# Kernel tuning notes

Measured on AMD Instinct MI355X. Metric: run time of the kernel, lower is better.

The kernel has to match this reference:

```python
import jax, jax.numpy as jnp
from jax import lax
import numpy as np

B = 16384
D = 32
N_HEADS = 4


def _piece_table():
    base = np.zeros((7, 4, 4), np.int32)
    cells = [
        [(1, 0), (1, 1), (1, 2), (1, 3)],  # I
        [(1, 1), (1, 2), (2, 1), (2, 2)],  # O
        [(1, 1), (2, 0), (2, 1), (2, 2)],  # T
        [(1, 1), (1, 2), (2, 0), (2, 1)],  # S
        [(1, 0), (1, 1), (2, 1), (2, 2)],  # Z
        [(1, 0), (2, 0), (2, 1), (2, 2)],  # J
        [(1, 2), (2, 0), (2, 1), (2, 2)],  # L
    ]
    for i, cs in enumerate(cells):
        for (r, c) in cs:
            base[i, r, c] = 1
    rots = np.stack([np.stack([np.rot90(base[i], k) for k in range(4)]) for i in range(7)])
    p = np.concatenate([rots, np.zeros((1, 4, 4, 4), np.int32)], 0)  # [8,4,4,4]
    return jnp.asarray(p)


def setup_inputs() -> dict:
    key = jax.random.key(0)
    ks = jax.random.split(key, 24)

    def ri(k, n, lo, hi):
        return jax.random.randint(k, (B, n), lo, hi, dtype=jnp.int32)

    t = jnp.concatenate([
        ri(ks[0], 1, 0, 10),   # col0 feature
        ri(ks[1], 1, 2, 8),
        ri(ks[2], 1, 0, 10),   # col2 y pos
        ri(ks[3], 1, 0, 8),    # col3 drop dist
        ri(ks[4], 1, 0, 4),    # col4 rotation
        ri(ks[5], 3, 0, 10),   # cols5-7
        ri(ks[6], 1, 0, 7),    # col8 piece id
        ri(ks[7], 6, 0, 7),    # cols9-14 hold/next
        ri(ks[8], 7, 0, 10),   # cols15-21
        ri(ks[9], 210, 0, 2),  # cols22-231 board
    ], axis=1)

    s = 0.05
    rn = lambda k, shp: jax.random.normal(k, shp, jnp.float32) * s
    return {
        "t": t,
        "piece_table": _piece_table(),
        "conv1_w": rn(ks[10], (6, 3, 5, 5)), "conv1_b": rn(ks[11], (6,)),
        "conv2_w": rn(ks[12], (16, 6, 5, 5)), "conv2_b": rn(ks[13], (16,)),
        "conv3_w": rn(ks[14], (64, 16, 3, 1)), "conv3_b": rn(ks[15], (64,)),
        "lfc1_w": rn(ks[16], (32, 64)), "lfc1_b": rn(ks[17], (32,)),
        "fc_w": rn(ks[18], (32, 8)), "fc_b": rn(ks[19], (32,)),
        "emb": rn(ks[20], (8, D)),
        "in_proj_w": rn(ks[21], (3 * D, D)), "in_proj_b": jnp.zeros((3 * D,), jnp.float32),
        "out_proj_w": rn(ks[22], (D, D)), "out_proj_b": jnp.zeros((D,), jnp.float32),
    }


def _avgpool2(x):
    b, c, h, w = x.shape
    h2, w2 = h // 2, w // 2
    return x[:, :, :h2 * 2, :w2 * 2].reshape(b, c, h2, 2, w2, 2).mean((3, 5))


def _lenet(x, w1, b1, w2, b2, w3, b3, fw, fb):
    dn = ("NCHW", "OIHW", "NCHW")
    x = jax.nn.relu(lax.conv_general_dilated(x, w1, (1, 1), ((2, 2), (2, 2)), dimension_numbers=dn) + b1[None, :, None, None])
    x = _avgpool2(x)                                   # [B,6,11,6]
    x = jax.nn.relu(lax.conv_general_dilated(x, w2, (1, 1), ((0, 0), (0, 0)), dimension_numbers=dn) + b2[None, :, None, None])
    x = _avgpool2(x)                                   # [B,16,3,1]
    x = jax.nn.relu(lax.conv_general_dilated(x, w3, (1, 1), ((0, 0), (0, 0)), dimension_numbers=dn) + b3[None, :, None, None])
    x = x.reshape(-1, 64)
    return jax.nn.relu(x @ fw.T + fb)                  # [B,32]


def _pe():
    pos = jnp.array([0, 0, 1, 2, 3, 4, 5], jnp.float32)[:, None]
    div = jnp.exp(jnp.arange(0, D, 2, dtype=jnp.float32) * (-jnp.log(10000.0) / D))
    s, c = jnp.sin(pos * div), jnp.cos(pos * div)      # [7,16] each
    return jnp.stack([s, c], -1).reshape(7, D)         # interleaved sin/cos


def _mha(q_in, kv, in_w, in_b, out_w, out_b):
    qw, kw, vw = in_w[:D], in_w[D:2 * D], in_w[2 * D:]
    qb, kb, vb = in_b[:D], in_b[D:2 * D], in_b[2 * D:]
    b, lq, _ = q_in.shape
    hd = D // N_HEADS
    q = (q_in @ qw.T + qb).reshape(b, lq, N_HEADS, hd)
    k = (kv @ kw.T + kb).reshape(b, -1, N_HEADS, hd)
    v = (kv @ vw.T + vb).reshape(b, -1, N_HEADS, hd)
    scores = jnp.einsum("bqhd,bkhd->bhqk", q, k) / jnp.sqrt(jnp.float32(hd))
    w = jax.nn.softmax(scores, axis=-1)
    o = jnp.einsum("bhqk,bkhd->bqhd", w, v).reshape(b, lq, D)
    return o @ out_w.T + out_b


def reference(t, piece_table, conv1_w, conv1_b, conv2_w, conv2_b, conv3_w, conv3_b,
              lfc1_w, lfc1_b, fc_w, fc_b, emb, in_proj_w, in_proj_b, out_proj_w, out_proj_b):
    bsz = t.shape[0]
    board = jnp.zeros((bsz, 3, 21, 10), jnp.float32)
    board = board.at[:, 0].set(t[:, 22:232].astype(jnp.float32).reshape(bsz, 21, 10))

    # gather piece grid, extract the 4 filled cells per sample in row-major order
    pieces = piece_table[t[:, 8], t[:, 4]].reshape(bsz, 16)        # [B,16] in {0,1}
    idx = jnp.argsort(1 - pieces, axis=1, stable=True)[:, :4]      # first 4 ones, scan order
    cy, cx = idx // 4, idx % 4
    x = cx + t[:, 1][:, None] - 2
    y = cy + t[:, 2][:, None]
    ny = y + t[:, 3][:, None]
    mask = (y >= 0) & (ny >= 0)
    br = jnp.arange(bsz, dtype=jnp.int32)[:, None]
    y_m = jnp.where(mask, y, -1)
    ny_m = jnp.where(mask, ny, -1)
    board = board.at[br, 1, y_m, x].set(1.0, mode="drop")
    board = board.at[br, 2, ny_m, x].set(1.0, mode="drop")

    board = jnp.pad(board, ((0, 0), (0, 0), (0, 1), (1, 1)), constant_values=1.0)  # [B,3,22,12]

    t9 = jnp.where((t[:, 9] != -1) & (t[:, 6] != 0), t[:, 9], 7)
    hold_next = jnp.concatenate([t[:, 8:9], t9[:, None], t[:, 10:15]], axis=1)     # [B,7]

    b2 = _lenet(board, conv1_w, conv1_b, conv2_w, conv2_b, conv3_w, conv3_b, lfc1_w, lfc1_b)  # [B,32]
    bkv = b2[:, None, :]                                            # [B,1,32]
    p = emb[hold_next] + _pe()[None]                                # [B,7,32]
    a = _mha(p, bkv, in_proj_w, in_proj_b, out_proj_w, out_proj_b)  # [B,7,32]

    xf = jax.nn.relu(t[:, :8].astype(jnp.float32) @ fc_w.T + fc_b)  # [B,32]
    out = jnp.concatenate([xf, a.mean(axis=1), b2], axis=1)         # [B,96]
    return (out, board)
```

## Files before the change

kernel.cpp:

```cpp
#include <hip/hip_runtime.h>
#include <cstddef>


#define BATCH 16384
#define SPB   4
#define NBLK  (BATCH / SPB)
#define SS    1804

__global__ __launch_bounds__(256, 4)
void board_model_kernel(const int* __restrict__ t,
                        const int* __restrict__ piece_table,
                        const float* __restrict__ w1, const float* __restrict__ b1,
                        const float* __restrict__ w2, const float* __restrict__ b2w,
                        const float* __restrict__ w3, const float* __restrict__ b3,
                        const float* __restrict__ wf1, const float* __restrict__ bf1,
                        const float* __restrict__ fcw, const float* __restrict__ fcb,
                        const float* __restrict__ ipw, const float* __restrict__ ipb,
                        const float* __restrict__ opw, const float* __restrict__ opb,
                        float* __restrict__ out,
                        float* __restrict__ out_board)
{
  __shared__ __align__(16) float scr[SPB * SS];

  const int tid  = threadIdx.x;
  const int lane = tid & 63;
  const int wv   = tid >> 6;
  const int bb   = blockIdx.x * SPB;

  {
    float* W = &scr[wv * SS];
    const int* tr = t + (size_t)(bb + wv) * 232;

    float4* W4 = (float4*)W;
    for (int i = lane; i < 351; i += 64) W4[i] = float4{0.f, 0.f, 0.f, 0.f};

    for (int i = lane; i < 210; i += 64) {
      int r = i / 10, b = i - r * 10;
      W[(r + 2) * 18 + b + 5] = (float)tr[22 + i];
    }

    for (int i = lane; i < 162; i += 64) {
      int ch = i / 54, k = i - ch * 54;
      int rr, cc;
      if (k < 12)      { rr = 23;         cc = k + 4; }
      else if (k < 33) { rr = k - 12 + 2; cc = 4; }
      else             { rr = k - 33 + 2; cc = 15; }
      W[ch * 468 + rr * 18 + cc] = 1.f;
    }

    if (lane < 4) {
      const int* pt = piece_table + (tr[8] * 4 + tr[4]) * 16;
      int sel = -1, n1 = 0;
#pragma unroll
      for (int j = 0; j < 16; ++j) { if (pt[j]) { if (n1 == lane) sel = j; ++n1; } }
      if (sel < 0) {
        int n0 = 0, want = lane - n1;
#pragma unroll
        for (int j = 0; j < 16; ++j) if (!pt[j]) { if (n0 == want) { sel = j; break; } ++n0; }
      }
      int cy = sel >> 2, cx = sel & 3;
      int x  = cx + tr[1] - 2;
      int y  = cy + tr[2];
      int ny = y + tr[3];
      if (y >= 0 && ny >= 0) {
        if (y  < 21 && x >= 0 && x < 10) W[468 + (y  + 2) * 18 + x + 5] = 1.f;
        if (ny < 21 && x >= 0 && x < 10) W[936 + (ny + 2) * 18 + x + 5] = 1.f;
      }
    }
    __builtin_amdgcn_wave_barrier();

    float* ob = out_board + (size_t)(bb + wv) * 792;
    for (int v = lane; v < 198; v += 64) {
      int j0 = v * 4;
      int ch = j0 / 264, rem = j0 - ch * 264;
      int r = rem / 12, c = rem - r * 12;
      const float* src = &W[ch * 468 + (r + 2) * 18 + c + 4];
      float4 val{src[0], src[1], src[2], src[3]};
      *(float4*)(ob + j0) = val;
    }
  }
  __syncthreads();

  {
    int g = tid;
    int q = g / 66, p = g - q * 66;
    int r = p / 6, c = p - r * 6;
    const float* base0 = &scr[q * SS] + (2 * r) * 18 + (2 * c + 2);
    float acc[2][2][6];
#pragma unroll
    for (int i = 0; i < 2; ++i)
#pragma unroll
      for (int j = 0; j < 2; ++j)
#pragma unroll
        for (int o = 0; o < 6; ++o) acc[i][j][o] = b1[o];

    for (int ic = 0; ic < 3; ++ic) {
      const float* base = base0 + ic * 468;
#pragma unroll
      for (int u = 0; u < 6; ++u) {
        float2 a0 = *(const float2*)(base + u * 18);
        float2 a1 = *(const float2*)(base + u * 18 + 2);
        float2 a2 = *(const float2*)(base + u * 18 + 4);
        float rv[6] = {a0.x, a0.y, a1.x, a1.y, a2.x, a2.y};
#pragma unroll
        for (int i = 0; i < 2; ++i) {
          if (u - i < 0 || u - i > 4) continue;
          const int ky = u - i;
#pragma unroll
          for (int j = 0; j < 2; ++j)
#pragma unroll
            for (int kx = 0; kx < 5; ++kx) {
              float xv = rv[j + kx];
#pragma unroll
              for (int o = 0; o < 6; ++o)
                acc[i][j][o] += xv * w1[((o * 3 + ic) * 5 + ky) * 5 + kx];
            }
        }
      }
    }
    float* P1q = &scr[q * SS + 1404];
#pragma unroll
    for (int o = 0; o < 6; ++o) {
      float v = fmaxf(acc[0][0][o], 0.f) + fmaxf(acc[0][1][o], 0.f)
              + fmaxf(acc[1][0][o], 0.f) + fmaxf(acc[1][1][o], 0.f);
      P1q[o * 66 + p] = 0.25f * v;
    }
  }

  if (tid < 32) {
    int pos = 58 + (tid >> 2), cell = tid & 3;
    int i2 = cell >> 1, j2 = cell & 1;
    int rp = pos / 6, cp = pos - rp * 6;
    int r2 = 2 * rp + i2, c2 = 2 * cp + j2;
    const float* Wq = &scr[3 * SS];
    float a6[6];
#pragma unroll
    for (int o = 0; o < 6; ++o) a6[o] = b1[o];
    for (int ic = 0; ic < 3; ++ic)
#pragma unroll
      for (int ky = 0; ky < 5; ++ky)
#pragma unroll
        for (int kx = 0; kx < 5; ++kx) {
          float xv = Wq[ic * 468 + (r2 + ky) * 18 + c2 + kx + 2];
#pragma unroll
          for (int o = 0; o < 6; ++o)
            a6[o] += xv * w1[((o * 3 + ic) * 5 + ky) * 5 + kx];
        }
#pragma unroll
    for (int o = 0; o < 6; ++o) {
      float v = fmaxf(a6[o], 0.f);
      v += __shfl_xor(v, 1, 64);
      v += __shfl_xor(v, 2, 64);
      a6[o] = v;
    }
    if (cell == 0) {
#pragma unroll
      for (int o = 0; o < 6; ++o)
        scr[3 * SS + 1404 + o * 66 + pos] = 0.25f * a6[o];
    }
  }
  __syncthreads();

  const int wvu = __builtin_amdgcn_readfirstlane(wv);

  if (lane < 48) {
    int q = lane / 12, p = lane - q * 12;
    int r = p >> 1, c = p & 1;
    const float* P1q = &scr[q * SS + 1404];
    float a4[4];
#pragma unroll
    for (int oo = 0; oo < 4; ++oo) a4[oo] = b2w[4 * wvu + oo];
    for (int ic = 0; ic < 6; ++ic)
#pragma unroll
      for (int kr = 0; kr < 5; ++kr) {
        float xv[5];
#pragma unroll
        for (int kc = 0; kc < 5; ++kc)
          xv[kc] = P1q[ic * 66 + (r + kr) * 6 + c + kc];
#pragma unroll
        for (int kc = 0; kc < 5; ++kc)
#pragma unroll
          for (int oo = 0; oo < 4; ++oo)
            a4[oo] += xv[kc] * w2[(((4 * wvu + oo) * 6 + ic) * 5 + kr) * 5 + kc];
      }
    float* C2q = &scr[q * SS];
#pragma unroll
    for (int oo = 0; oo < 4; ++oo)
      C2q[(4 * wvu + oo) * 12 + p] = fmaxf(a4[oo], 0.f);
  }
  __syncthreads();

  {
    const int q = wvu;
    float* S = &scr[q * SS];

    if (lane < 48) {
      int o = lane / 3, pr = lane - o * 3;
      float v = 0.25f * (S[o * 12 + 4 * pr] + S[o * 12 + 4 * pr + 1]
                       + S[o * 12 + 4 * pr + 2] + S[o * 12 + 4 * pr + 3]);
      S[192 + lane] = v;
    }
    __builtin_amdgcn_wave_barrier();

    {
      int o = lane;
      float acc = b3[o];
#pragma unroll
      for (int k = 0; k < 48; ++k) acc += S[192 + k] * w3[o * 48 + k];
      S[240 + o] = fmaxf(acc, 0.f);
    }
    __builtin_amdgcn_wave_barrier();

    {
      int j = lane & 31, h = lane >> 5;
      float part = 0.f;
#pragma unroll
      for (int kk = 0; kk < 32; ++kk) {
        int k = 32 * h + kk;
        part += S[240 + k] * wf1[j * 64 + k];
      }
      part += __shfl_xor(part, 32, 64);
      if (h == 0) {
        float acc = fmaxf(bf1[j] + part, 0.f);
        S[304 + j] = acc;
        out[(size_t)(bb + q) * 96 + 64 + j] = acc;
      }
    }
    __builtin_amdgcn_wave_barrier();

    {
      int j = lane & 31;
      if (lane < 32) {
        float acc = ipb[64 + j];
#pragma unroll
        for (int k = 0; k < 32; ++k) acc += S[304 + k] * ipw[(64 + j) * 32 + k];
        S[336 + j] = acc;
      } else {
        const int* tr = t + (size_t)(bb + q) * 232;
        float acc = fcb[j];
#pragma unroll
        for (int k = 0; k < 8; ++k) acc += (float)tr[k] * fcw[j * 8 + k];
        out[(size_t)(bb + q) * 96 + j] = fmaxf(acc, 0.f);
      }
    }
    __builtin_amdgcn_wave_barrier();

    if (lane < 32) {
      int j = lane;
      float acc = opb[j];
#pragma unroll
      for (int k = 0; k < 32; ++k) acc += S[336 + k] * opw[j * 32 + k];
      out[(size_t)(bb + q) * 96 + 32 + j] = acc;
    }
  }
}

extern "C" void kernel_launch(void* const* d_in, const int* in_sizes, int n_in,
                              void* d_out, int out_size, void* d_ws, size_t ws_size,
                              hipStream_t stream) {
  const int*   t   = (const int*)d_in[0];
  const int*   pt  = (const int*)d_in[1];
  const float* w1  = (const float*)d_in[2];
  const float* b1  = (const float*)d_in[3];
  const float* w2  = (const float*)d_in[4];
  const float* b2w = (const float*)d_in[5];
  const float* w3  = (const float*)d_in[6];
  const float* b3  = (const float*)d_in[7];
  const float* wf1 = (const float*)d_in[8];
  const float* bf1 = (const float*)d_in[9];
  const float* fcw = (const float*)d_in[10];
  const float* fcb = (const float*)d_in[11];
  const float* ipw = (const float*)d_in[13];
  const float* ipb = (const float*)d_in[14];
  const float* opw = (const float*)d_in[15];
  const float* opb = (const float*)d_in[16];

  float* out       = (float*)d_out;
  float* out_board = out + (size_t)BATCH * 96;

  hipLaunchKernelGGL(board_model_kernel, dim3(NBLK), dim3(256), 0, stream,
                     t, pt, w1, b1, w2, b2w, w3, b3, wf1, bf1, fcw, fcb,
                     ipw, ipb, opw, opb, out, out_board);
}
```

Baseline: 202.4 us.

## Use odd LDS row stride, interleave pool1 channels, raise occupancy hint

Changes the shared-memory board row stride from 18 to 17 and the channel stride to 442, and stores pooled conv1 outputs position-major with stride 7 instead of channel-major. The conv2 loop is reordered so that each input position's channels are read together. The aim is fewer LDS bank conflicts, plus a smaller per-sample footprint that allows launch_bounds to request 5 blocks per CU instead of 4. The cost is that the float2 vector loads are replaced with scalar LDS loads, and the tighter register budget could cause spills.

```diff
diff --git a/kernel.cpp b/kernel.cpp
--- a/kernel.cpp
+++ b/kernel.cpp
@@ -5,9 +5,12 @@
 #define BATCH 16384
 #define SPB   4
 #define NBLK  (BATCH / SPB)
-#define SS    1804
-
-__global__ __launch_bounds__(256, 4)
+#define RS    17
+#define CHS   442
+#define P1OFF 1328
+#define SS    1800
+
+__global__ __launch_bounds__(256, 5)
 void board_model_kernel(const int* __restrict__ t,
                         const int* __restrict__ piece_table,
                         const float* __restrict__ w1, const float* __restrict__ b1,
@@ -32,11 +35,11 @@
     const int* tr = t + (size_t)(bb + wv) * 232;
 
     float4* W4 = (float4*)W;
-    for (int i = lane; i < 351; i += 64) W4[i] = float4{0.f, 0.f, 0.f, 0.f};
+    for (int i = lane; i < 332; i += 64) W4[i] = float4{0.f, 0.f, 0.f, 0.f};
 
     for (int i = lane; i < 210; i += 64) {
       int r = i / 10, b = i - r * 10;
-      W[(r + 2) * 18 + b + 5] = (float)tr[22 + i];
+      W[(r + 2) * RS + b + 5] = (float)tr[22 + i];
     }
 
     for (int i = lane; i < 162; i += 64) {
@@ -45,7 +48,7 @@
       if (k < 12)      { rr = 23;         cc = k + 4; }
       else if (k < 33) { rr = k - 12 + 2; cc = 4; }
       else             { rr = k - 33 + 2; cc = 15; }
-      W[ch * 468 + rr * 18 + cc] = 1.f;
+      W[ch * CHS + rr * RS + cc] = 1.f;
     }
 
     if (lane < 4) {
@@ -63,8 +66,8 @@
       int y  = cy + tr[2];
       int ny = y + tr[3];
       if (y >= 0 && ny >= 0) {
-        if (y  < 21 && x >= 0 && x < 10) W[468 + (y  + 2) * 18 + x + 5] = 1.f;
-        if (ny < 21 && x >= 0 && x < 10) W[936 + (ny + 2) * 18 + x + 5] = 1.f;
+        if (y  < 21 && x >= 0 && x < 10) W[CHS     + (y  + 2) * RS + x + 5] = 1.f;
+        if (ny < 21 && x >= 0 && x < 10) W[2 * CHS + (ny + 2) * RS + x + 5] = 1.f;
       }
     }
     __builtin_amdgcn_wave_barrier();
@@ -74,7 +77,7 @@
       int j0 = v * 4;
       int ch = j0 / 264, rem = j0 - ch * 264;
       int r = rem / 12, c = rem - r * 12;
-      const float* src = &W[ch * 468 + (r + 2) * 18 + c + 4];
+      const float* src = &W[ch * CHS + (r + 2) * RS + c + 4];
       float4 val{src[0], src[1], src[2], src[3]};
       *(float4*)(ob + j0) = val;
     }
@@ -85,7 +88,7 @@
     int g = tid;
     int q = g / 66, p = g - q * 66;
     int r = p / 6, c = p - r * 6;
-    const float* base0 = &scr[q * SS] + (2 * r) * 18 + (2 * c + 2);
+    const float* base0 = &scr[q * SS] + (2 * r) * RS + (2 * c + 2);
     float acc[2][2][6];
 #pragma unroll
     for (int i = 0; i < 2; ++i)
@@ -95,13 +98,12 @@
         for (int o = 0; o < 6; ++o) acc[i][j][o] = b1[o];
 
     for (int ic = 0; ic < 3; ++ic) {
-      const float* base = base0 + ic * 468;
+      const float* base = base0 + ic * CHS;
 #pragma unroll
       for (int u = 0; u < 6; ++u) {
-        float2 a0 = *(const float2*)(base + u * 18);
-        float2 a1 = *(const float2*)(base + u * 18 + 2);
-        float2 a2 = *(const float2*)(base + u * 18 + 4);
-        float rv[6] = {a0.x, a0.y, a1.x, a1.y, a2.x, a2.y};
+        float rv[6];
+#pragma unroll
+        for (int x = 0; x < 6; ++x) rv[x] = base[u * RS + x];
 #pragma unroll
         for (int i = 0; i < 2; ++i) {
           if (u - i < 0 || u - i > 4) continue;
@@ -118,12 +120,12 @@
         }
       }
     }
-    float* P1q = &scr[q * SS + 1404];
+    float* P1q = &scr[q * SS + P1OFF];
 #pragma unroll
     for (int o = 0; o < 6; ++o) {
       float v = fmaxf(acc[0][0][o], 0.f) + fmaxf(acc[0][1][o], 0.f)
               + fmaxf(acc[1][0][o], 0.f) + fmaxf(acc[1][1][o], 0.f);
-      P1q[o * 66 + p] = 0.25f * v;
+      P1q[p * 7 + o] = 0.25f * v;
     }
   }
 
@@ -141,7 +143,7 @@
       for (int ky = 0; ky < 5; ++ky)
 #pragma unroll
         for (int kx = 0; kx < 5; ++kx) {
-          float xv = Wq[ic * 468 + (r2 + ky) * 18 + c2 + kx + 2];
+          float xv = Wq[ic * CHS + (r2 + ky) * RS + c2 + kx + 2];
 #pragma unroll
           for (int o = 0; o < 6; ++o)
             a6[o] += xv * w1[((o * 3 + ic) * 5 + ky) * 5 + kx];
@@ -156,7 +158,7 @@
     if (cell == 0) {
 #pragma unroll
       for (int o = 0; o < 6; ++o)
-        scr[3 * SS + 1404 + o * 66 + pos] = 0.25f * a6[o];
+        scr[3 * SS + P1OFF + pos * 7 + o] = 0.25f * a6[o];
     }
   }
   __syncthreads();
@@ -166,22 +168,23 @@
   if (lane < 48) {
     int q = lane / 12, p = lane - q * 12;
     int r = p >> 1, c = p & 1;
-    const float* P1q = &scr[q * SS + 1404];
+    const float* P1q = &scr[q * SS + P1OFF];
     float a4[4];
 #pragma unroll
     for (int oo = 0; oo < 4; ++oo) a4[oo] = b2w[4 * wvu + oo];
-    for (int ic = 0; ic < 6; ++ic)
-#pragma unroll
-      for (int kr = 0; kr < 5; ++kr) {
-        float xv[5];
-#pragma unroll
-        for (int kc = 0; kc < 5; ++kc)
-          xv[kc] = P1q[ic * 66 + (r + kr) * 6 + c + kc];
-#pragma unroll
-        for (int kc = 0; kc < 5; ++kc)
+#pragma unroll
+    for (int kr = 0; kr < 5; ++kr)
+#pragma unroll
+      for (int kc = 0; kc < 5; ++kc) {
+        const float* pv = &P1q[((r + kr) * 6 + (c + kc)) * 7];
+        float rv[6];
+#pragma unroll
+        for (int ic = 0; ic < 6; ++ic) rv[ic] = pv[ic];
+#pragma unroll
+        for (int ic = 0; ic < 6; ++ic)
 #pragma unroll
           for (int oo = 0; oo < 4; ++oo)
-            a4[oo] += xv[kc] * w2[(((4 * wvu + oo) * 6 + ic) * 5 + kr) * 5 + kc];
+            a4[oo] += rv[ic] * w2[(((4 * wvu + oo) * 6 + ic) * 5 + kr) * 5 + kc];
       }
     float* C2q = &scr[q * SS];
 #pragma unroll
```

New measurement: 426.6 us. +110.8%, slower.

## Split conv stage and batched MLP tail into two kernels, rebalance conv1 leftovers

Applied to the files above, without the earlier changes.

Splits the fused kernel in two. The conv kernel now writes pooled conv2 features to a workspace buffer. A new tail kernel runs conv3, the linear layers, attention value/out projections and the fc branch with one sample per lane, keeping weights uniform across the wave and the activations in registers. The leftover conv1 positions for sample 3 are now spread over all four waves with 16-lane reductions instead of a single half-wave. This trades a workspace round trip and an extra launch for removing the serial per-sample tail work from the conv kernel and dropping the 4-wave occupancy bound.

```diff
diff --git a/kernel.cpp b/kernel.cpp
--- a/kernel.cpp
+++ b/kernel.cpp
@@ -5,20 +5,17 @@
 #define BATCH 16384
 #define SPB   4
 #define NBLK  (BATCH / SPB)
+#define RS    18
+#define CHS   468
 #define SS    1804
 
-__global__ __launch_bounds__(256, 4)
-void board_model_kernel(const int* __restrict__ t,
-                        const int* __restrict__ piece_table,
-                        const float* __restrict__ w1, const float* __restrict__ b1,
-                        const float* __restrict__ w2, const float* __restrict__ b2w,
-                        const float* __restrict__ w3, const float* __restrict__ b3,
-                        const float* __restrict__ wf1, const float* __restrict__ bf1,
-                        const float* __restrict__ fcw, const float* __restrict__ fcb,
-                        const float* __restrict__ ipw, const float* __restrict__ ipb,
-                        const float* __restrict__ opw, const float* __restrict__ opb,
-                        float* __restrict__ out,
-                        float* __restrict__ out_board)
+__global__ __launch_bounds__(256)
+void board_conv_kernel(const int* __restrict__ t,
+                       const int* __restrict__ piece_table,
+                       const float* __restrict__ w1, const float* __restrict__ b1,
+                       const float* __restrict__ w2, const float* __restrict__ b2w,
+                       float* __restrict__ p2g,
+                       float* __restrict__ out_board)
 {
   __shared__ __align__(16) float scr[SPB * SS];
 
@@ -36,7 +33,7 @@
 
     for (int i = lane; i < 210; i += 64) {
       int r = i / 10, b = i - r * 10;
-      W[(r + 2) * 18 + b + 5] = (float)tr[22 + i];
+      W[(r + 2) * RS + b + 5] = (float)tr[22 + i];
     }
 
     for (int i = lane; i < 162; i += 64) {
@@ -45,7 +42,7 @@
       if (k < 12)      { rr = 23;         cc = k + 4; }
       else if (k < 33) { rr = k - 12 + 2; cc = 4; }
       else             { rr = k - 33 + 2; cc = 15; }
-      W[ch * 468 + rr * 18 + cc] = 1.f;
+      W[ch * CHS + rr * RS + cc] = 1.f;
     }
 
     if (lane < 4) {
@@ -63,8 +60,8 @@
       int y  = cy + tr[2];
       int ny = y + tr[3];
       if (y >= 0 && ny >= 0) {
-        if (y  < 21 && x >= 0 && x < 10) W[468 + (y  + 2) * 18 + x + 5] = 1.f;
-        if (ny < 21 && x >= 0 && x < 10) W[936 + (ny + 2) * 18 + x + 5] = 1.f;
+        if (y  < 21 && x >= 0 && x < 10) W[CHS     + (y  + 2) * RS + x + 5] = 1.f;
+        if (ny < 21 && x >= 0 && x < 10) W[2 * CHS + (ny + 2) * RS + x + 5] = 1.f;
       }
     }
     __builtin_amdgcn_wave_barrier();
@@ -74,7 +71,7 @@
       int j0 = v * 4;
       int ch = j0 / 264, rem = j0 - ch * 264;
       int r = rem / 12, c = rem - r * 12;
-      const float* src = &W[ch * 468 + (r + 2) * 18 + c + 4];
+      const float* src = &W[ch * CHS + (r + 2) * RS + c + 4];
       float4 val{src[0], src[1], src[2], src[3]};
       *(float4*)(ob + j0) = val;
     }
@@ -85,7 +82,7 @@
     int g = tid;
     int q = g / 66, p = g - q * 66;
     int r = p / 6, c = p - r * 6;
-    const float* base0 = &scr[q * SS] + (2 * r) * 18 + (2 * c + 2);
+    const float* base0 = &scr[q * SS] + (2 * r) * RS + (2 * c + 2);
     float acc[2][2][6];
 #pragma unroll
     for (int i = 0; i < 2; ++i)
@@ -95,12 +92,12 @@
         for (int o = 0; o < 6; ++o) acc[i][j][o] = b1[o];
 
     for (int ic = 0; ic < 3; ++ic) {
-      const float* base = base0 + ic * 468;
+      const float* base = base0 + ic * CHS;
 #pragma unroll
       for (int u = 0; u < 6; ++u) {
-        float2 a0 = *(const float2*)(base + u * 18);
-        float2 a1 = *(const float2*)(base + u * 18 + 2);
-        float2 a2 = *(const float2*)(base + u * 18 + 4);
+        float2 a0 = *(const float2*)(base + u * RS);
+        float2 a1 = *(const float2*)(base + u * RS + 2);
+        float2 a2 = *(const float2*)(base + u * RS + 4);
         float rv[6] = {a0.x, a0.y, a1.x, a1.y, a2.x, a2.y};
 #pragma unroll
         for (int i = 0; i < 2; ++i) {
@@ -127,36 +124,47 @@
     }
   }
 
-  if (tid < 32) {
-    int pos = 58 + (tid >> 2), cell = tid & 3;
-    int i2 = cell >> 1, j2 = cell & 1;
-    int rp = pos / 6, cp = pos - rp * 6;
-    int r2 = 2 * rp + i2, c2 = 2 * cp + j2;
-    const float* Wq = &scr[3 * SS];
-    float a6[6];
-#pragma unroll
-    for (int o = 0; o < 6; ++o) a6[o] = b1[o];
-    for (int ic = 0; ic < 3; ++ic)
-#pragma unroll
-      for (int ky = 0; ky < 5; ++ky)
-#pragma unroll
-        for (int kx = 0; kx < 5; ++kx) {
-          float xv = Wq[ic * 468 + (r2 + ky) * 18 + c2 + kx + 2];
+  {
+    const int g16 = lane >> 4;
+    const int kl  = lane & 15;
+    const float* Wq3 = &scr[3 * SS];
+    float psum[6] = {0.f, 0.f, 0.f, 0.f, 0.f, 0.f};
+#pragma unroll
+    for (int cc2 = 0; cc2 < 2; ++cc2) {
+      int cell = (wv * 4 + g16) * 2 + cc2;
+      int pos  = 58 + (cell >> 2);
+      int sub  = cell & 3;
+      int rp = pos / 6, cp = pos - rp * 6;
+      int r2 = 2 * rp + (sub >> 1), c2 = 2 * cp + (sub & 1);
+      float a6[6] = {0.f, 0.f, 0.f, 0.f, 0.f, 0.f};
+#pragma unroll
+      for (int it = 0; it < 5; ++it) {
+        int k = kl + 16 * it;
+        if (k < 75) {
+          int ic = k / 25, rem = k - ic * 25;
+          int ky = rem / 5, kx = rem - ky * 5;
+          float xv = Wq3[ic * CHS + (r2 + ky) * RS + (c2 + kx + 2)];
 #pragma unroll
           for (int o = 0; o < 6; ++o)
             a6[o] += xv * w1[((o * 3 + ic) * 5 + ky) * 5 + kx];
         }
-#pragma unroll
-    for (int o = 0; o < 6; ++o) {
-      float v = fmaxf(a6[o], 0.f);
-      v += __shfl_xor(v, 1, 64);
-      v += __shfl_xor(v, 2, 64);
-      a6[o] = v;
-    }
-    if (cell == 0) {
+      }
+#pragma unroll
+      for (int o = 0; o < 6; ++o) {
+        float v = a6[o];
+        v += __shfl_xor(v, 1, 64);  v += __shfl_xor(v, 2, 64);
+        v += __shfl_xor(v, 4, 64);  v += __shfl_xor(v, 8, 64);
+        psum[o] += fmaxf(v + b1[o], 0.f);
+      }
+    }
+#pragma unroll
+    for (int o = 0; o < 6; ++o)
+      psum[o] += __shfl_xor(psum[o], 16, 64);
+    if (kl == 0 && (g16 & 1) == 0) {
+      int pos = 58 + wv * 2 + (g16 >> 1);
 #pragma unroll
       for (int o = 0; o < 6; ++o)
-        scr[3 * SS + 1404 + o * 66 + pos] = 0.25f * a6[o];
+        scr[3 * SS + 1404 + o * 66 + pos] = 0.25f * psum[o];
     }
   }
   __syncthreads();
@@ -190,68 +198,103 @@
   }
   __syncthreads();
 
+  if (lane < 48) {
+    const int q = wvu;
+    const float* C2q = &scr[q * SS];
+    int o = lane / 3, pr = lane - o * 3;
+    float v = 0.25f * (C2q[o * 12 + 4 * pr] + C2q[o * 12 + 4 * pr + 1]
+                     + C2q[o * 12 + 4 * pr + 2] + C2q[o * 12 + 4 * pr + 3]);
+    p2g[(size_t)(bb + q) * 48 + lane] = v;
+  }
+}
+
+__global__ __launch_bounds__(64)
+void tail_kernel(const int* __restrict__ t,
+                 const float* __restrict__ p2g,
+                 const float* __restrict__ w3, const float* __restrict__ b3,
+                 const float* __restrict__ wf1, const float* __restrict__ bf1,
+                 const float* __restrict__ fcw, const float* __restrict__ fcb,
+                 const float* __restrict__ ipw, const float* __restrict__ ipb,
+                 const float* __restrict__ opw, const float* __restrict__ opb,
+                 float* __restrict__ out)
+{
+  __shared__ float P2L[64 * 49];
+  __shared__ float C3L[64 * 64];
+  __shared__ float OUTL[64 * 97];
+
+  const int lane = threadIdx.x;
+  const int s0   = blockIdx.x * 64;
+
+  for (int idx = lane; idx < 3072; idx += 64) {
+    int s = idx / 48, k = idx - s * 48;
+    P2L[s * 49 + k] = p2g[(size_t)s0 * 48 + idx];
+  }
+  __builtin_amdgcn_wave_barrier();
+
+  float p2[48];
+#pragma unroll
+  for (int k = 0; k < 48; ++k) p2[k] = P2L[lane * 49 + k];
+
+  for (int o = 0; o < 64; ++o) {
+    float acc = b3[o];
+#pragma unroll
+    for (int k = 0; k < 48; ++k) acc += p2[k] * w3[o * 48 + k];
+    C3L[o * 64 + lane] = fmaxf(acc, 0.f);
+  }
+  __builtin_amdgcn_wave_barrier();
+
+  float c3[64];
+#pragma unroll
+  for (int k = 0; k < 64; ++k) c3[k] = C3L[k * 64 + lane];
+
+  for (int j = 0; j < 32; ++j) {
+    float acc = bf1[j];
+#pragma unroll
+    for (int k = 0; k < 64; ++k) acc += c3[k] * wf1[j * 64 + k];
+    OUTL[lane * 97 + 64 + j] = fmaxf(acc, 0.f);
+  }
+  __builtin_amdgcn_wave_barrier();
+
+  float b2r[32];
+#pragma unroll
+  for (int k = 0; k < 32; ++k) b2r[k] = OUTL[lane * 97 + 64 + k];
+
+  for (int j = 0; j < 32; ++j) {
+    float acc = ipb[64 + j];
+#pragma unroll
+    for (int k = 0; k < 32; ++k) acc += b2r[k] * ipw[(64 + j) * 32 + k];
+    C3L[j * 64 + lane] = acc;
+  }
+  __builtin_amdgcn_wave_barrier();
+
+  float vr[32];
+#pragma unroll
+  for (int k = 0; k < 32; ++k) vr[k] = C3L[k * 64 + lane];
+
+  for (int j = 0; j < 32; ++j) {
+    float acc = opb[j];
+#pragma unroll
+    for (int k = 0; k < 32; ++k) acc += vr[k] * opw[j * 32 + k];
+    OUTL[lane * 97 + 32 + j] = acc;
+  }
+
   {
-    const int q = wvu;
-    float* S = &scr[q * SS];
-
-    if (lane < 48) {
-      int o = lane / 3, pr = lane - o * 3;
-      float v = 0.25f * (S[o * 12 + 4 * pr] + S[o * 12 + 4 * pr + 1]
-                       + S[o * 12 + 4 * pr + 2] + S[o * 12 + 4 * pr + 3]);
-      S[192 + lane] = v;
-    }
-    __builtin_amdgcn_wave_barrier();
-
-    {
-      int o = lane;
-      float acc = b3[o];
-#pragma unroll
-      for (int k = 0; k < 48; ++k) acc += S[192 + k] * w3[o * 48 + k];
-      S[240 + o] = fmaxf(acc, 0.f);
-    }
-    __builtin_amdgcn_wave_barrier();
-
-    {
-      int j = lane & 31, h = lane >> 5;
-      float part = 0.f;
-#pragma unroll
-      for (int kk = 0; kk < 32; ++kk) {
-        int k = 32 * h + kk;
-        part += S[240 + k] * wf1[j * 64 + k];
-      }
-      part += __shfl_xor(part, 32, 64);
-      if (h == 0) {
-        float acc = fmaxf(bf1[j] + part, 0.f);
-        S[304 + j] = acc;
-        out[(size_t)(bb + q) * 96 + 64 + j] = acc;
-      }
-    }
-    __builtin_amdgcn_wave_barrier();
-
-    {
-      int j = lane & 31;
-      if (lane < 32) {
-        float acc = ipb[64 + j];
-#pragma unroll
-        for (int k = 0; k < 32; ++k) acc += S[304 + k] * ipw[(64 + j) * 32 + k];
-        S[336 + j] = acc;
-      } else {
-        const int* tr = t + (size_t)(bb + q) * 232;
-        float acc = fcb[j];
-#pragma unroll
-        for (int k = 0; k < 8; ++k) acc += (float)tr[k] * fcw[j * 8 + k];
-        out[(size_t)(bb + q) * 96 + j] = fmaxf(acc, 0.f);
-      }
-    }
-    __builtin_amdgcn_wave_barrier();
-
-    if (lane < 32) {
-      int j = lane;
-      float acc = opb[j];
-#pragma unroll
-      for (int k = 0; k < 32; ++k) acc += S[336 + k] * opw[j * 32 + k];
-      out[(size_t)(bb + q) * 96 + 32 + j] = acc;
-    }
+    const int* tr = t + (size_t)(s0 + lane) * 232;
+    float tf[8];
+#pragma unroll
+    for (int k = 0; k < 8; ++k) tf[k] = (float)tr[k];
+    for (int j = 0; j < 32; ++j) {
+      float acc = fcb[j];
+#pragma unroll
+      for (int k = 0; k < 8; ++k) acc += tf[k] * fcw[j * 8 + k];
+      OUTL[lane * 97 + j] = fmaxf(acc, 0.f);
+    }
+  }
+  __builtin_amdgcn_wave_barrier();
+
+  for (int idx = lane; idx < 6144; idx += 64) {
+    int s = idx / 96, j = idx - s * 96;
+    out[(size_t)s0 * 96 + idx] = OUTL[s * 97 + j];
   }
 }
 
@@ -277,8 +320,10 @@
 
   float* out       = (float*)d_out;
   float* out_board = out + (size_t)BATCH * 96;
-
-  hipLaunchKernelGGL(board_model_kernel, dim3(NBLK), dim3(256), 0, stream,
-                     t, pt, w1, b1, w2, b2w, w3, b3, wf1, bf1, fcw, fcb,
-                     ipw, ipb, opw, opb, out, out_board);
+  float* p2g       = (float*)d_ws;
+
+  hipLaunchKernelGGL(board_conv_kernel, dim3(NBLK), dim3(256), 0, stream,
+                     t, pt, w1, b1, w2, b2w, p2g, out_board);
+  hipLaunchKernelGGL(tail_kernel, dim3(BATCH / 64), dim3(64), 0, stream,
+                     t, p2g, w3, b3, wf1, bf1, fcw, fcb, ipw, ipb, opw, opb, out);
 }
```

Result: slower. 298.1 us (+47.3%).

## Exploit sparse conv1 channels via precomputed border contribution and piece-cell scatter

Applied to the files above, without the earlier changes.

Conv1 is split into a dense pass over the board channel only. The constant padding border's contribution is precomputed per output position by a small prelaunch kernel. The two piece channels, which hold at most four ones each, are added as a sparse scatter of weight entries. This removes two thirds of the conv1 MACs and shrinks shared memory per sample. It also stages w1 and the border table in LDS and spreads the remainder positions across all waves. The cost is an extra kernel launch, more LDS for the tables, and divergent branches in the sparse update.

```diff
diff --git a/kernel.cpp b/kernel.cpp
--- a/kernel.cpp
+++ b/kernel.cpp
@@ -5,9 +5,33 @@
 #define BATCH 16384
 #define SPB   4
 #define NBLK  (BATCH / SPB)
-#define SS    1804
-
-__global__ __launch_bounds__(256, 4)
+#define RS    18
+#define SS2   884
+
+__global__ __launch_bounds__(256)
+void cborder_kernel(const float* __restrict__ w1, float* __restrict__ cb)
+{
+  int i = blockIdx.x * 256 + threadIdx.x;
+  if (i >= 1584) return;
+  int p = i / 6, o = i - p * 6;
+  int y0 = p / 12, x0 = p - y0 * 12;
+  float acc = 0.f;
+#pragma unroll
+  for (int dy = 0; dy < 5; ++dy)
+#pragma unroll
+    for (int dx = 0; dx < 5; ++dx) {
+      int pr = y0 + dy - 2, pc = x0 + dx - 2;
+      if (pr >= 0 && pr < 22 && pc >= 0 && pc < 12 &&
+          (pr == 21 || pc == 0 || pc == 11)) {
+        int k = dy * 5 + dx;
+        acc += w1[(o * 3 + 0) * 25 + k] + w1[(o * 3 + 1) * 25 + k]
+             + w1[(o * 3 + 2) * 25 + k];
+      }
+    }
+  cb[p * 6 + o] = acc;
+}
+
+__global__ __launch_bounds__(256)
 void board_model_kernel(const int* __restrict__ t,
                         const int* __restrict__ piece_table,
                         const float* __restrict__ w1, const float* __restrict__ b1,
@@ -17,35 +41,33 @@
                         const float* __restrict__ fcw, const float* __restrict__ fcb,
                         const float* __restrict__ ipw, const float* __restrict__ ipb,
                         const float* __restrict__ opw, const float* __restrict__ opb,
+                        const float* __restrict__ cbg,
                         float* __restrict__ out,
                         float* __restrict__ out_board)
 {
-  __shared__ __align__(16) float scr[SPB * SS];
+  __shared__ __align__(16) float scr[SPB * SS2];
+  __shared__ float w1L[450];
+  __shared__ float cbL[1584];
 
   const int tid  = threadIdx.x;
   const int lane = tid & 63;
   const int wv   = tid >> 6;
   const int bb   = blockIdx.x * SPB;
 
+  for (int i = tid; i < 450; i += 256) w1L[i] = w1[i];
+  for (int i = tid; i < 1584; i += 256) cbL[i] = cbg[i];
+
   {
-    float* W = &scr[wv * SS];
+    float* W = &scr[wv * SS2];
+    int*   pcs = (int*)&scr[wv * SS2 + 864];
     const int* tr = t + (size_t)(bb + wv) * 232;
 
     float4* W4 = (float4*)W;
-    for (int i = lane; i < 351; i += 64) W4[i] = float4{0.f, 0.f, 0.f, 0.f};
+    for (int i = lane; i < 117; i += 64) W4[i] = float4{0.f, 0.f, 0.f, 0.f};
 
     for (int i = lane; i < 210; i += 64) {
       int r = i / 10, b = i - r * 10;
-      W[(r + 2) * 18 + b + 5] = (float)tr[22 + i];
-    }
-
-    for (int i = lane; i < 162; i += 64) {
-      int ch = i / 54, k = i - ch * 54;
-      int rr, cc;
-      if (k < 12)      { rr = 23;         cc = k + 4; }
-      else if (k < 33) { rr = k - 12 + 2; cc = 4; }
-      else             { rr = k - 33 + 2; cc = 15; }
-      W[ch * 468 + rr * 18 + cc] = 1.f;
+      W[(r + 2) * RS + b + 5] = (float)tr[22 + i];
     }
 
     if (lane < 4) {
@@ -62,10 +84,14 @@
       int x  = cx + tr[1] - 2;
       int y  = cy + tr[2];
       int ny = y + tr[3];
-      if (y >= 0 && ny >= 0) {
-        if (y  < 21 && x >= 0 && x < 10) W[468 + (y  + 2) * 18 + x + 5] = 1.f;
-        if (ny < 21 && x >= 0 && x < 10) W[936 + (ny + 2) * 18 + x + 5] = 1.f;
-      }
+      bool mask = (y >= 0) && (ny >= 0);
+      bool xok  = (x >= 0) && (x < 10);
+      bool v1 = mask && xok && (y < 21);
+      bool v2 = mask && xok && (ny < 21);
+      pcs[2 * lane + 0]     = v1 ? y  : -100;
+      pcs[2 * lane + 1]     = x + 1;
+      pcs[2 * (lane + 4)]   = v2 ? ny : -100;
+      pcs[2 * (lane + 4) + 1] = x + 1;
     }
     __builtin_amdgcn_wave_barrier();
 
@@ -74,9 +100,28 @@
       int j0 = v * 4;
       int ch = j0 / 264, rem = j0 - ch * 264;
       int r = rem / 12, c = rem - r * 12;
-      const float* src = &W[ch * 468 + (r + 2) * 18 + c + 4];
-      float4 val{src[0], src[1], src[2], src[3]};
-      *(float4*)(ob + j0) = val;
+      float val[4];
+      if (ch == 0) {
+#pragma unroll
+        for (int d = 0; d < 4; ++d) {
+          int cd = c + d;
+          val[d] = (r == 21 || cd == 0 || cd == 11) ? 1.f
+                 : W[(r + 2) * RS + cd + 4];
+        }
+      } else {
+#pragma unroll
+        for (int d = 0; d < 4; ++d) {
+          int cd = c + d;
+          val[d] = (r == 21 || cd == 0 || cd == 11) ? 1.f : 0.f;
+        }
+#pragma unroll
+        for (int e = 0; e < 4; ++e) {
+          int pr = pcs[2 * ((ch - 1) * 4 + e)];
+          int pc = pcs[2 * ((ch - 1) * 4 + e) + 1];
+          if (pr == r && (unsigned)(pc - c) < 4u) val[pc - c] = 1.f;
+        }
+      }
+      *(float4*)(ob + j0) = float4{val[0], val[1], val[2], val[3]};
     }
   }
   __syncthreads();
@@ -85,22 +130,26 @@
     int g = tid;
     int q = g / 66, p = g - q * 66;
     int r = p / 6, c = p - r * 6;
-    const float* base0 = &scr[q * SS] + (2 * r) * 18 + (2 * c + 2);
+    const float* Wq  = &scr[q * SS2];
+    const int*   pcs = (const int*)&scr[q * SS2 + 864];
     float acc[2][2][6];
 #pragma unroll
     for (int i = 0; i < 2; ++i)
 #pragma unroll
-      for (int j = 0; j < 2; ++j)
-#pragma unroll
-        for (int o = 0; o < 6; ++o) acc[i][j][o] = b1[o];
-
-    for (int ic = 0; ic < 3; ++ic) {
-      const float* base = base0 + ic * 468;
+      for (int j = 0; j < 2; ++j) {
+        int pcell = (2 * r + i) * 12 + (2 * c + j);
+#pragma unroll
+        for (int o = 0; o < 6; ++o)
+          acc[i][j][o] = b1[o] + cbL[pcell * 6 + o];
+      }
+
+    {
+      const float* base = Wq + (2 * r) * RS + (2 * c + 2);
 #pragma unroll
       for (int u = 0; u < 6; ++u) {
-        float2 a0 = *(const float2*)(base + u * 18);
-        float2 a1 = *(const float2*)(base + u * 18 + 2);
-        float2 a2 = *(const float2*)(base + u * 18 + 4);
+        float2 a0 = *(const float2*)(base + u * RS);
+        float2 a1 = *(const float2*)(base + u * RS + 2);
+        float2 a2 = *(const float2*)(base + u * RS + 4);
         float rv[6] = {a0.x, a0.y, a1.x, a1.y, a2.x, a2.y};
 #pragma unroll
         for (int i = 0; i < 2; ++i) {
@@ -113,12 +162,37 @@
               float xv = rv[j + kx];
 #pragma unroll
               for (int o = 0; o < 6; ++o)
-                acc[i][j][o] += xv * w1[((o * 3 + ic) * 5 + ky) * 5 + kx];
+                acc[i][j][o] += xv * w1L[o * 75 + ky * 5 + kx];
             }
         }
       }
     }
-    float* P1q = &scr[q * SS + 1404];
+
+#pragma unroll
+    for (int e = 0; e < 8; ++e) {
+      int pr = pcs[2 * e];
+      if (pr < 0) continue;
+      int pc = pcs[2 * e + 1];
+      int ch = 1 + (e >> 2);
+      int dyb = pr + 2 - 2 * r;
+      int dxb = pc + 2 - 2 * c;
+      if (dyb < 0 || dyb > 5 || dxb < 0 || dxb > 5) continue;
+#pragma unroll
+      for (int i = 0; i < 2; ++i) {
+        int dy = dyb - i;
+        if ((unsigned)dy >= 5u) continue;
+#pragma unroll
+        for (int j = 0; j < 2; ++j) {
+          int dx = dxb - j;
+          if ((unsigned)dx >= 5u) continue;
+#pragma unroll
+          for (int o = 0; o < 6; ++o)
+            acc[i][j][o] += w1L[o * 75 + ch * 25 + dy * 5 + dx];
+        }
+      }
+    }
+
+    float* P1q = &scr[q * SS2 + 468];
 #pragma unroll
     for (int o = 0; o < 6; ++o) {
       float v = fmaxf(acc[0][0][o], 0.f) + fmaxf(acc[0][1][o], 0.f)
@@ -127,36 +201,63 @@
     }
   }
 
-  if (tid < 32) {
-    int pos = 58 + (tid >> 2), cell = tid & 3;
-    int i2 = cell >> 1, j2 = cell & 1;
-    int rp = pos / 6, cp = pos - rp * 6;
-    int r2 = 2 * rp + i2, c2 = 2 * cp + j2;
-    const float* Wq = &scr[3 * SS];
-    float a6[6];
-#pragma unroll
-    for (int o = 0; o < 6; ++o) a6[o] = b1[o];
-    for (int ic = 0; ic < 3; ++ic)
-#pragma unroll
-      for (int ky = 0; ky < 5; ++ky)
-#pragma unroll
-        for (int kx = 0; kx < 5; ++kx) {
-          float xv = Wq[ic * 468 + (r2 + ky) * 18 + c2 + kx + 2];
+  {
+    const int g16 = lane >> 4;
+    const int kl  = lane & 15;
+    const float* W3b  = &scr[3 * SS2];
+    const int*   pcs3 = (const int*)&scr[3 * SS2 + 864];
+    float psum[6] = {0.f, 0.f, 0.f, 0.f, 0.f, 0.f};
+#pragma unroll
+    for (int cc2 = 0; cc2 < 2; ++cc2) {
+      int cell = (wv * 4 + g16) * 2 + cc2;
+      int pos  = 58 + (cell >> 2);
+      int sub  = cell & 3;
+      int rp = pos / 6, cp = pos - rp * 6;
+      int y0 = 2 * rp + (sub >> 1), x0 = 2 * cp + (sub & 1);
+      float a6[6] = {0.f, 0.f, 0.f, 0.f, 0.f, 0.f};
+#pragma unroll
+      for (int it = 0; it < 2; ++it) {
+        int k = kl + 16 * it;
+        if (k < 25) {
+          int dy = k / 5, dx = k - dy * 5;
+          float xv = W3b[(y0 + dy) * RS + x0 + dx + 2];
 #pragma unroll
           for (int o = 0; o < 6; ++o)
-            a6[o] += xv * w1[((o * 3 + ic) * 5 + ky) * 5 + kx];
-        }
-#pragma unroll
-    for (int o = 0; o < 6; ++o) {
-      float v = fmaxf(a6[o], 0.f);
-      v += __shfl_xor(v, 1, 64);
-      v += __shfl_xor(v, 2, 64);
-      a6[o] = v;
-    }
-    if (cell == 0) {
+            a6[o] += xv * w1L[o * 75 + dy * 5 + dx];
+        }
+      }
+#pragma unroll
+      for (int o = 0; o < 6; ++o) {
+        float v = a6[o];
+        v += __shfl_xor(v, 1, 64);  v += __shfl_xor(v, 2, 64);
+        v += __shfl_xor(v, 4, 64);  v += __shfl_xor(v, 8, 64);
+        a6[o] = v + b1[o] + cbL[(y0 * 12 + x0) * 6 + o];
+      }
+#pragma unroll
+      for (int e = 0; e < 8; ++e) {
+        int pr = pcs3[2 * e];
+        if (pr < 0) continue;
+        int pc = pcs3[2 * e + 1];
+        int ch = 1 + (e >> 2);
+        int dy = pr + 2 - y0;
+        int dx = pc + 2 - x0;
+        if ((unsigned)dy < 5u && (unsigned)dx < 5u) {
+#pragma unroll
+          for (int o = 0; o < 6; ++o)
+            a6[o] += w1L[o * 75 + ch * 25 + dy * 5 + dx];
+        }
+      }
+#pragma unroll
+      for (int o = 0; o < 6; ++o) psum[o] += fmaxf(a6[o], 0.f);
+    }
+#pragma unroll
+    for (int o = 0; o < 6; ++o)
+      psum[o] += __shfl_xor(psum[o], 16, 64);
+    if (kl == 0 && (g16 & 1) == 0) {
+      int pos = 58 + wv * 2 + (g16 >> 1);
 #pragma unroll
       for (int o = 0; o < 6; ++o)
-        scr[3 * SS + 1404 + o * 66 + pos] = 0.25f * a6[o];
+        scr[3 * SS2 + 468 + o * 66 + pos] = 0.25f * psum[o];
     }
   }
   __syncthreads();
@@ -166,7 +267,7 @@
   if (lane < 48) {
     int q = lane / 12, p = lane - q * 12;
     int r = p >> 1, c = p & 1;
-    const float* P1q = &scr[q * SS + 1404];
+    const float* P1q = &scr[q * SS2 + 468];
     float a4[4];
 #pragma unroll
     for (int oo = 0; oo < 4; ++oo) a4[oo] = b2w[4 * wvu + oo];
@@ -183,7 +284,7 @@
           for (int oo = 0; oo < 4; ++oo)
             a4[oo] += xv[kc] * w2[(((4 * wvu + oo) * 6 + ic) * 5 + kr) * 5 + kc];
       }
-    float* C2q = &scr[q * SS];
+    float* C2q = &scr[q * SS2];
 #pragma unroll
     for (int oo = 0; oo < 4; ++oo)
       C2q[(4 * wvu + oo) * 12 + p] = fmaxf(a4[oo], 0.f);
@@ -192,7 +293,7 @@
 
   {
     const int q = wvu;
-    float* S = &scr[q * SS];
+    float* S = &scr[q * SS2];
 
     if (lane < 48) {
       int o = lane / 3, pr = lane - o * 3;
@@ -277,8 +378,10 @@
 
   float* out       = (float*)d_out;
   float* out_board = out + (size_t)BATCH * 96;
-
+  float* cbg       = (float*)d_ws;
+
+  hipLaunchKernelGGL(cborder_kernel, dim3(7), dim3(256), 0, stream, w1, cbg);
   hipLaunchKernelGGL(board_model_kernel, dim3(NBLK), dim3(256), 0, stream,
                      t, pt, w1, b1, w2, b2w, w3, b3, wf1, bf1, fcw, fcb,
-                     ipw, ipb, opw, opb, out, out_board);
+                     ipw, ipb, opw, opb, cbg, out, out_board);
 }
```

Measured after the change: 250.0 us. +23.5%, slower.
